# Optimization experiments

Measured on AMD Instinct MI355X. Metric: run time of the kernel, lower is better.

## Reference

```python
import jax, jax.numpy as jnp
import numpy as np

HC = 4
C = 2048
TMAX = 8
RMS_EPS = 1e-6
PRE_EPS = 1e-4
SINK_EPS = 1e-6
POST_MULT = 2.0


def setup_inputs() -> dict:
    key = jax.random.key(0)
    k1, k2, k3 = jax.random.split(key, 3)
    B, S = 2, 2048
    x = jax.random.normal(k1, (B, S, HC, C), dtype=jnp.float32)
    phi = jax.random.normal(k2, (HC * C, HC * HC + 2 * HC), dtype=jnp.float32) * 0.02
    b = jnp.zeros((HC * HC + 2 * HC,), dtype=jnp.float32)
    alpha_pre = jnp.ones((), dtype=jnp.float32)
    alpha_post = jnp.ones((), dtype=jnp.float32)
    alpha_res = jnp.ones((), dtype=jnp.float32)
    W = jax.random.normal(k3, (C, C), dtype=jnp.float32) * 0.02
    Wb = jnp.zeros((C,), dtype=jnp.float32)
    return {"x": x, "phi": phi, "b": b, "alpha_pre": alpha_pre,
            "alpha_post": alpha_post, "alpha_res": alpha_res, "W": W, "Wb": Wb}


def _coeffs(x, phi, b, alpha_pre, alpha_post, alpha_res):
    # x: [..., hc, c] -> flatten streams, RMSNorm over k = hc*c
    lead = x.shape[:-2]
    flat = x.reshape(lead + (HC * C,))
    xn = flat * jax.lax.rsqrt(jnp.mean(flat * flat, axis=-1, keepdims=True) + RMS_EPS)
    logits = xn @ phi + b  # [..., hc*hc + 2*hc]
    pre = logits[..., :HC]
    post = logits[..., HC:2 * HC]
    res = logits[..., 2 * HC:].reshape(lead + (HC, HC))
    h_pre = jax.nn.sigmoid(alpha_pre * pre) + PRE_EPS          # [..., hc]
    h_post = POST_MULT * jax.nn.sigmoid(alpha_post * post)     # [..., hc]
    # Sinkhorn normalization -> approximately doubly-stochastic hc x hc matrix
    M = jnp.exp(alpha_res * res)

    def step(m, _):
        m = m / (jnp.sum(m, axis=-1, keepdims=True) + SINK_EPS)
        m = m / (jnp.sum(m, axis=-2, keepdims=True) + SINK_EPS)
        return m, None

    h_res, _ = jax.lax.scan(step, M, None, length=TMAX)
    return h_pre, h_post, h_res


def reference(x, phi, b, alpha_pre, alpha_post, alpha_res, W, Wb):
    xf = x.astype(jnp.float32)
    h_pre, h_post, h_res = _coeffs(xf, phi, b, alpha_pre, alpha_post, alpha_res)
    # combine streams into single layer input: [..., c]
    x_in = jnp.sum(xf * h_pre[..., None], axis=-2)
    f_out = x_in @ W + Wb  # the wrapped layer (Linear)
    # residual stream mixing + broadcasted post-scaled layer output
    x_out = jnp.einsum('...oi,...ic->...oc', h_res, xf) + h_post[..., None] * f_out[..., None, :]
    return x_out.astype(x.dtype)
```

## Files before the change

kernel.cpp:

```cpp
#include <hip/hip_runtime.h>
#include <hip/hip_bf16.h>

#define HCn 4
#define Cn 2048
#define Dn (HCn*Cn)
#define NLg 24
#define TMAXn 8

typedef short bf16x8 __attribute__((ext_vector_type(8)));
typedef float f32x4 __attribute__((ext_vector_type(4)));

__device__ __forceinline__ unsigned int pk2(float a, float b) {
  union { __hip_bfloat162 h; unsigned int u; } v;
  v.h = __float22bfloat162_rn(float2{a, b});
  return v.u;
}
__device__ __forceinline__ unsigned short f2bfu(float a) {
  union { __hip_bfloat16 h; unsigned short u; } v;
  v.h = __float2bfloat16(a);
  return v.u;
}
__device__ __forceinline__ float bf2f(unsigned int u16) {
  union { float f; unsigned int x; } v;
  v.x = u16 << 16;
  return v.f;
}
__device__ __forceinline__ float sigm(float z) { return 1.0f / (1.0f + expf(-z)); }

__device__ __forceinline__ void gload_lds16(const void* g, void* l) {
  __builtin_amdgcn_global_load_lds((__attribute__((address_space(1))) void*)(g),
                                   (__attribute__((address_space(3))) void*)(l),
                                   16, 0, 0);
}

__global__ __launch_bounds__(128) void phib_kernel(const float* __restrict__ phi,
                                                   unsigned short* __restrict__ phiB) {
  int tid = threadIdx.x;
  int nt = tid >> 6, lane = tid & 63;
  int ks = blockIdx.x;
  int col = nt * 16 + (lane & 15);
  int kb = ks * 32 + (lane >> 4) * 8;
  float v[8];
#pragma unroll
  for (int e = 0; e < 8; ++e)
    v[e] = (col < NLg) ? phi[(size_t)(kb + e) * NLg + col] : 0.f;
  uint4 o = { pk2(v[0], v[1]), pk2(v[2], v[3]), pk2(v[4], v[5]), pk2(v[6], v[7]) };
  *(uint4*)&phiB[((size_t)(ks * 2 + nt) * 64 + lane) * 8] = o;
}

__global__ __launch_bounds__(512) void logits_kernel(
    const float* __restrict__ x, const unsigned short* __restrict__ phiB,
    float* __restrict__ pbuf) {
  __shared__ float lgp[8][16][33];
  __shared__ float ssp[8][16];

  int tid = threadIdx.x, lane = tid & 63, wid = tid >> 6;
  int g = blockIdx.x >> 2;
  int kc = blockIdx.x & 3;
  long t0 = (long)g * 16;
  int l15 = lane & 15, kg = lane >> 4;

  int kbase = kc * 2048 + wid * 256;
  const float* xr = x + (size_t)(t0 + l15) * Dn + kbase + kg * 8;
  const bf16x8* pB = (const bf16x8*)phiB + (size_t)(kbase >> 5) * 128 + lane;

  float ss = 0.f;
  f32x4 acc0 = {0.f,0.f,0.f,0.f}, acc1 = {0.f,0.f,0.f,0.f};

  float4 A0[3], A1[3]; bf16x8 Bv0[3], Bv1[3];
#define LOADIT(IT, S) {                          \
    A0[S] = *(const float4*)(xr + (IT) * 32);    \
    A1[S] = *(const float4*)(xr + (IT) * 32 + 4);\
    Bv0[S] = pB[(IT) * 128];                     \
    Bv1[S] = pB[(IT) * 128 + 64]; }
#define PROCIT(S) {                                                           \
    float4 P0 = A0[S], P1 = A1[S];                                            \
    ss += P0.x*P0.x + P0.y*P0.y + P0.z*P0.z + P0.w*P0.w;                      \
    ss += P1.x*P1.x + P1.y*P1.y + P1.z*P1.z + P1.w*P1.w;                      \
    uint4 u_ = { pk2(P0.x,P0.y), pk2(P0.z,P0.w), pk2(P1.x,P1.y), pk2(P1.z,P1.w) }; \
    bf16x8 a_ = *(bf16x8*)&u_;                                                \
    acc0 = __builtin_amdgcn_mfma_f32_16x16x32_bf16(a_, Bv0[S], acc0, 0, 0, 0);\
    acc1 = __builtin_amdgcn_mfma_f32_16x16x32_bf16(a_, Bv1[S], acc1, 0, 0, 0); }

  LOADIT(0, 0); LOADIT(1, 1);
#pragma unroll
  for (int it = 0; it < 8; ++it) {
    if (it < 6) LOADIT(it + 2, (it + 2) % 3);
    PROCIT(it % 3);
  }
#undef LOADIT
#undef PROCIT

  ss += __shfl_xor(ss, 16); ss += __shfl_xor(ss, 32);
  if (kg == 0) ssp[wid][l15] = ss;
#pragma unroll
  for (int e = 0; e < 4; ++e) {
    int tok = kg * 4 + e;
    lgp[wid][tok][l15] = acc0[e];
    lgp[wid][tok][16 + l15] = acc1[e];
  }
  __syncthreads();

  for (int q = tid; q < 16 * 25; q += 512) {
    int tk = q / 25, j = q % 25;
    float v = 0.f;
    if (j < 24) {
#pragma unroll
      for (int w = 0; w < 8; ++w) v += lgp[w][tk][j];
    } else {
#pragma unroll
      for (int w = 0; w < 8; ++w) v += ssp[w][tk];
    }
    pbuf[(size_t)(t0 + tk) * 100 + kc * 25 + j] = v;
  }
}

__global__ __launch_bounds__(256) void finalize_kernel(
    const float* __restrict__ pbuf, const float* __restrict__ bb,
    const float* __restrict__ apre_p, const float* __restrict__ apost_p,
    const float* __restrict__ ares_p, float* __restrict__ hpre,
    float* __restrict__ hpost, float* __restrict__ hres) {
  long t = (long)blockIdx.x * 256 + threadIdx.x;
  const float* pt = pbuf + (size_t)t * 100;
  float lg[25];
#pragma unroll
  for (int j = 0; j < 25; ++j)
    lg[j] = pt[j] + pt[25 + j] + pt[50 + j] + pt[75 + j];
  float r = rsqrtf(lg[24] / (float)Dn + 1e-6f);
  float apre = apre_p[0], apost = apost_p[0], ares = ares_p[0];
#pragma unroll
  for (int j = 0; j < NLg; ++j) lg[j] = r * lg[j] + bb[j];
#pragma unroll
  for (int j = 0; j < 4; ++j) hpre[t * 4 + j] = sigm(apre * lg[j]) + 1e-4f;
#pragma unroll
  for (int j = 0; j < 4; ++j) hpost[t * 4 + j] = 2.0f * sigm(apost * lg[4 + j]);
  float m[16];
#pragma unroll
  for (int q = 0; q < 16; ++q) m[q] = expf(ares * lg[8 + q]);
  for (int it = 0; it < TMAXn; ++it) {
#pragma unroll
    for (int o = 0; o < 4; ++o) {
      float rs = m[o*4] + m[o*4+1] + m[o*4+2] + m[o*4+3] + 1e-6f;
      m[o*4] /= rs; m[o*4+1] /= rs; m[o*4+2] /= rs; m[o*4+3] /= rs;
    }
#pragma unroll
    for (int i = 0; i < 4; ++i) {
      float cs = m[i] + m[4+i] + m[8+i] + m[12+i] + 1e-6f;
      m[i] /= cs; m[4+i] /= cs; m[8+i] /= cs; m[12+i] /= cs;
    }
  }
#pragma unroll
  for (int q = 0; q < 16; ++q) hres[t * 16 + q] = m[q];
}

__global__ __launch_bounds__(256) void xin_kernel(
    const float* __restrict__ x, const float* __restrict__ hpre,
    unsigned int* __restrict__ xin) {
  long t = blockIdx.x;
  int tid = threadIdx.x;
  float h0 = hpre[t * 4 + 0], h1 = hpre[t * 4 + 1];
  float h2 = hpre[t * 4 + 2], h3 = hpre[t * 4 + 3];
  const float4* xt = (const float4*)(x + (size_t)t * Dn);
  uint2* xo = (uint2*)xin + (size_t)t * (Cn / 4);
#pragma unroll
  for (int it = 0; it < 2; ++it) {
    int c4 = it * 256 + tid;
    float4 v0 = xt[c4];
    float4 v1 = xt[c4 + 512];
    float4 v2 = xt[c4 + 1024];
    float4 v3 = xt[c4 + 1536];
    float sx = h0*v0.x + h1*v1.x + h2*v2.x + h3*v3.x;
    float sy = h0*v0.y + h1*v1.y + h2*v2.y + h3*v3.y;
    float sz = h0*v0.z + h1*v1.z + h2*v2.z + h3*v3.z;
    float sw = h0*v0.w + h1*v1.w + h2*v2.w + h3*v3.w;
    uint2 o; o.x = pk2(sx, sy); o.y = pk2(sz, sw);
    xo[c4] = o;
  }
}

__global__ __launch_bounds__(256) void wtrans_kernel(const float* __restrict__ W,
                                                     unsigned short* __restrict__ Wt) {
  __shared__ float tile[64][65];
  int kb = blockIdx.y * 64, nb = blockIdx.x * 64;
  int tr = threadIdx.x >> 4;
  int tc = threadIdx.x & 15;
#pragma unroll
  for (int rr = 0; rr < 64; rr += 16) {
    float4 v = *(const float4*)&W[(size_t)(kb + tr + rr) * Cn + nb + tc * 4];
    tile[tr + rr][tc * 4 + 0] = v.x; tile[tr + rr][tc * 4 + 1] = v.y;
    tile[tr + rr][tc * 4 + 2] = v.z; tile[tr + rr][tc * 4 + 3] = v.w;
  }
  __syncthreads();
#pragma unroll
  for (int rr = 0; rr < 64; rr += 16) {
    int n = nb + tr + rr;
    uint2 o;
    o.x = pk2(tile[tc * 4 + 0][tr + rr], tile[tc * 4 + 1][tr + rr]);
    o.y = pk2(tile[tc * 4 + 2][tr + rr], tile[tc * 4 + 3][tr + rr]);
    *(uint2*)&Wt[(size_t)n * Cn + kb + tc * 4] = o;
  }
}

#define BMt 128
#define BNt 128
#define BKt 64
#define GK Cn
__global__ __launch_bounds__(256) void gemm_kernel(
    const unsigned short* __restrict__ xin, const unsigned short* __restrict__ Wt,
    const float* __restrict__ Wb, unsigned short* __restrict__ f) {
  __shared__ __align__(16) unsigned short As[2][BMt * BKt];
  __shared__ __align__(16) unsigned short Bs[2][BNt * BKt];
  int tid = threadIdx.x;
  int lane = tid & 63, wid = tid >> 6;
  int wr = wid >> 1, wc = wid & 1;
  int l15 = lane & 15, kg = lane >> 4;
  int wg = blockIdx.x;
  wg = (wg & 7) * 64 + (wg >> 3);
  int bx = wg & 15, by = wg >> 4;

  f32x4 acc[4][4];
#pragma unroll
  for (int i = 0; i < 4; ++i)
#pragma unroll
    for (int j = 0; j < 4; ++j) acc[i][j] = {0.f, 0.f, 0.f, 0.f};

  const char* Ab = (const char*)xin + (size_t)by * BMt * (GK * 2);
  const char* Bb = (const char*)Wt + (size_t)bx * BNt * (GK * 2);

  int soff[4]; size_t sgl[4];
#pragma unroll
  for (int i = 0; i < 4; ++i) {
    int off = tid * 16 + i * 4096;
    int row = off >> 7, col = off & 127;
    int scol = col ^ ((row & 7) << 4);
    soff[i] = off;
    sgl[i] = (size_t)row * (GK * 2) + scol;
  }
#define STAGEG(BUF, K0) {                                                      \
    _Pragma("unroll")                                                          \
    for (int i_ = 0; i_ < 4; ++i_)                                             \
      gload_lds16(Ab + sgl[i_] + (size_t)(K0) * 2, (char*)As[BUF] + soff[i_]); \
    _Pragma("unroll")                                                          \
    for (int i_ = 0; i_ < 4; ++i_)                                             \
      gload_lds16(Bb + sgl[i_] + (size_t)(K0) * 2, (char*)Bs[BUF] + soff[i_]); }

  int aoff[4][2], boff[4][2];
#pragma unroll
  for (int fm = 0; fm < 4; ++fm) {
    int ar = wr * 64 + fm * 16 + l15;
    int br = wc * 64 + fm * 16 + l15;
#pragma unroll
    for (int ks = 0; ks < 2; ++ks) {
      int c = ks * 64 + kg * 16;
      aoff[fm][ks] = ar * 128 + (c ^ ((ar & 7) << 4));
      boff[fm][ks] = br * 128 + (c ^ ((br & 7) << 4));
    }
  }

  STAGEG(0, 0);
  asm volatile("s_waitcnt vmcnt(0)" ::: "memory");
  __builtin_amdgcn_s_barrier();

  for (int t = 0; t < GK / BKt; ++t) {
    int cur = t & 1;
    if (t < GK / BKt - 1) STAGEG(cur ^ 1, (t + 1) * BKt);
#pragma unroll
    for (int ks = 0; ks < 2; ++ks) {
      bf16x8 av[4], bv[4];
#pragma unroll
      for (int fm = 0; fm < 4; ++fm)
        av[fm] = *(const bf16x8*)((const char*)As[cur] + aoff[fm][ks]);
#pragma unroll
      for (int fn = 0; fn < 4; ++fn)
        bv[fn] = *(const bf16x8*)((const char*)Bs[cur] + boff[fn][ks]);
#pragma unroll
      for (int fm = 0; fm < 4; ++fm)
#pragma unroll
        for (int fn = 0; fn < 4; ++fn)
          acc[fm][fn] = __builtin_amdgcn_mfma_f32_16x16x32_bf16(av[fm], bv[fn], acc[fm][fn], 0, 0, 0);
    }
    asm volatile("s_waitcnt vmcnt(0)" ::: "memory");
    __builtin_amdgcn_s_barrier();
  }

  int m0 = by * BMt + wr * 64;
  int n0 = bx * BNt + wc * 64;
#pragma unroll
  for (int fm = 0; fm < 4; ++fm) {
#pragma unroll
    for (int e = 0; e < 4; ++e) {
      int t = m0 + fm * 16 + kg * 4 + e;
      unsigned short* ft = f + (size_t)t * Cn;
#pragma unroll
      for (int fn = 0; fn < 4; ++fn) {
        int c = n0 + fn * 16 + l15;
        ft[c] = f2bfu(acc[fm][fn][e] + Wb[c]);
      }
    }
  }
}

__global__ __launch_bounds__(256) void epilogue_kernel(
    const float* __restrict__ x, const unsigned short* __restrict__ f,
    const float* __restrict__ hpost, const float* __restrict__ hres,
    float* __restrict__ out) {
  long t = blockIdx.x;
  int tid = threadIdx.x;
  float hq[4], hr[16];
#pragma unroll
  for (int o = 0; o < 4; ++o) hq[o] = hpost[t * 4 + o];
#pragma unroll
  for (int q = 0; q < 16; ++q) hr[q] = hres[t * 16 + q];
  const float4* xt = (const float4*)(x + (size_t)t * Dn);
  const uint2* ft = (const uint2*)(f + (size_t)t * Cn);
  float* ot = out + (size_t)t * Dn;
#pragma unroll
  for (int it = 0; it < 2; ++it) {
    int c4 = it * 256 + tid;
    float4 x0 = xt[c4], x1 = xt[c4 + 512], x2 = xt[c4 + 1024], x3 = xt[c4 + 1536];
    uint2 fu = ft[c4];
    float4 fv = { bf2f(fu.x & 0xffffu), bf2f(fu.x >> 16),
                  bf2f(fu.y & 0xffffu), bf2f(fu.y >> 16) };
#pragma unroll
    for (int o = 0; o < 4; ++o) {
      float a = hr[o*4+0], b = hr[o*4+1], c = hr[o*4+2], d = hr[o*4+3], q = hq[o];
      f32x4 r;
      r[0] = q*fv.x + a*x0.x + b*x1.x + c*x2.x + d*x3.x;
      r[1] = q*fv.y + a*x0.y + b*x1.y + c*x2.y + d*x3.y;
      r[2] = q*fv.z + a*x0.z + b*x1.z + c*x2.z + d*x3.z;
      r[3] = q*fv.w + a*x0.w + b*x1.w + c*x2.w + d*x3.w;
      __builtin_nontemporal_store(r, (f32x4*)&ot[(size_t)o * Cn + c4 * 4]);
    }
  }
}

extern "C" void kernel_launch(void* const* d_in, const int* in_sizes, int n_in,
                              void* d_out, int out_size, void* d_ws, size_t ws_size,
                              hipStream_t stream) {
  const float* x     = (const float*)d_in[0];
  const float* phi   = (const float*)d_in[1];
  const float* b     = (const float*)d_in[2];
  const float* apre  = (const float*)d_in[3];
  const float* apost = (const float*)d_in[4];
  const float* ares  = (const float*)d_in[5];
  const float* W     = (const float*)d_in[6];
  const float* Wb    = (const float*)d_in[7];
  float* out = (float*)d_out;

  int NT = in_sizes[0] / Dn;
  char* ws = (char*)d_ws;
  size_t off = 0;
  unsigned int*   xin  = (unsigned int*)(ws + off);   off += (size_t)NT * Cn * 2;
  unsigned short* Wt   = (unsigned short*)(ws + off); off += (size_t)Cn * Cn * 2;
  float* hpre  = (float*)(ws + off); off += (size_t)NT * 4 * 4;
  float* hpost = (float*)(ws + off); off += (size_t)NT * 4 * 4;
  float* hres  = (float*)(ws + off); off += (size_t)NT * 16 * 4;
  unsigned short* phiB = (unsigned short*)(ws + off); off += (size_t)Dn * 32 * 2;
  float* pbuf  = (float*)(ws + off); off += (size_t)NT * 100 * 4;
  unsigned short* fbuf = (unsigned short*)(ws + off); off += (size_t)NT * Cn * 2;

  hipLaunchKernelGGL(phib_kernel, dim3(Dn / 32), dim3(128), 0, stream, phi, phiB);
  hipLaunchKernelGGL(logits_kernel, dim3((NT / 16) * 4), dim3(512), 0, stream,
                     x, phiB, pbuf);
  hipLaunchKernelGGL(finalize_kernel, dim3(NT / 256), dim3(256), 0, stream,
                     pbuf, b, apre, apost, ares, hpre, hpost, hres);
  hipLaunchKernelGGL(xin_kernel, dim3(NT), dim3(256), 0, stream, x, hpre, xin);
  hipLaunchKernelGGL(wtrans_kernel, dim3(Cn / 64, Cn / 64), dim3(256), 0, stream, W, Wt);
  hipLaunchKernelGGL(gemm_kernel, dim3((Cn / BNt) * (NT / BMt)), dim3(256), 0, stream,
                     (const unsigned short*)xin, Wt, Wb, fbuf);
  hipLaunchKernelGGL(epilogue_kernel, dim3(NT), dim3(256), 0, stream,
                     x, fbuf, hpost, hres, out);
}
```

Before: 164.2 us.

## Stage x tiles through LDS with async global-to-LDS loads in logits kernel

The logits kernel now moves x into a per-wave double-buffered LDS area using direct global-to-LDS 16-byte loads, instead of prefetching into registers three stages deep. It synchronises with explicit vmcnt/lgkmcnt waits and scheduling barriers. All eight phi fragments are loaded into registers up front rather than streamed alongside x. The aim is to cut register pressure and keep more memory traffic in flight while the bf16 conversion and MFMA run. In exchange it adds an LDS round trip, hand-written wait counts that must match the load order, and extra registers for the preloaded B fragments.

```diff
diff --git a/kernel.cpp b/kernel.cpp
--- a/kernel.cpp
+++ b/kernel.cpp
@@ -51,6 +51,7 @@
 __global__ __launch_bounds__(512) void logits_kernel(
     const float* __restrict__ x, const unsigned short* __restrict__ phiB,
     float* __restrict__ pbuf) {
+  __shared__ __align__(16) float Axs[8][2][512];
   __shared__ float lgp[8][16][33];
   __shared__ float ssp[8][16];
 
@@ -58,44 +59,62 @@
   int g = blockIdx.x >> 2;
   int kc = blockIdx.x & 3;
   long t0 = (long)g * 16;
-  int l15 = lane & 15, kg = lane >> 4;
-
-  int kbase = kc * 2048 + wid * 256;
-  const float* xr = x + (size_t)(t0 + l15) * Dn + kbase + kg * 8;
-  const bf16x8* pB = (const bf16x8*)phiB + (size_t)(kbase >> 5) * 128 + lane;
+  int l15 = lane & 15, sg = lane >> 4;
+
+  int kwin = kc * 2048 + wid * 256;
+  const float* xs = x + (size_t)(t0 + l15) * Dn + kwin + sg * 8;
+  const bf16x8* pB = (const bf16x8*)phiB + (size_t)(kwin >> 5) * 128 + lane;
+
+  float* A0 = &Axs[wid][0][0];
+  float* A1 = &Axs[wid][1][0];
+
+  bf16x8 Bv0[8], Bv1[8];
+#pragma unroll
+  for (int it = 0; it < 8; ++it) {
+    Bv0[it] = pB[it * 128];
+    Bv1[it] = pB[it * 128 + 64];
+  }
+
+#define STAGE(IT, BUF) {                                                 \
+    gload_lds16(xs + (IT) * 32,     (char*)(BUF) + lane * 16);           \
+    gload_lds16(xs + (IT) * 32 + 4, (char*)(BUF) + 1024 + lane * 16); }
+
+  int rb0 = l15 * 16 + sg * 256;
+  int rb1 = rb0 + 1024;
 
   float ss = 0.f;
   f32x4 acc0 = {0.f,0.f,0.f,0.f}, acc1 = {0.f,0.f,0.f,0.f};
 
-  float4 A0[3], A1[3]; bf16x8 Bv0[3], Bv1[3];
-#define LOADIT(IT, S) {                          \
-    A0[S] = *(const float4*)(xr + (IT) * 32);    \
-    A1[S] = *(const float4*)(xr + (IT) * 32 + 4);\
-    Bv0[S] = pB[(IT) * 128];                     \
-    Bv1[S] = pB[(IT) * 128 + 64]; }
-#define PROCIT(S) {                                                           \
-    float4 P0 = A0[S], P1 = A1[S];                                            \
-    ss += P0.x*P0.x + P0.y*P0.y + P0.z*P0.z + P0.w*P0.w;                      \
-    ss += P1.x*P1.x + P1.y*P1.y + P1.z*P1.z + P1.w*P1.w;                      \
-    uint4 u_ = { pk2(P0.x,P0.y), pk2(P0.z,P0.w), pk2(P1.x,P1.y), pk2(P1.z,P1.w) }; \
-    bf16x8 a_ = *(bf16x8*)&u_;                                                \
-    acc0 = __builtin_amdgcn_mfma_f32_16x16x32_bf16(a_, Bv0[S], acc0, 0, 0, 0);\
-    acc1 = __builtin_amdgcn_mfma_f32_16x16x32_bf16(a_, Bv1[S], acc1, 0, 0, 0); }
-
-  LOADIT(0, 0); LOADIT(1, 1);
+  STAGE(0, A0);
+  STAGE(1, A1);
 #pragma unroll
   for (int it = 0; it < 8; ++it) {
-    if (it < 6) LOADIT(it + 2, (it + 2) % 3);
-    PROCIT(it % 3);
-  }
-#undef LOADIT
-#undef PROCIT
+    float* cb = (it & 1) ? A1 : A0;
+    if (it < 7) {
+      asm volatile("s_waitcnt vmcnt(2)" ::: "memory");
+    } else {
+      asm volatile("s_waitcnt vmcnt(0)" ::: "memory");
+    }
+    __builtin_amdgcn_sched_barrier(0);
+    float4 a0 = *(const float4*)((const char*)cb + rb0);
+    float4 a1 = *(const float4*)((const char*)cb + rb1);
+    asm volatile("s_waitcnt lgkmcnt(0)" ::: "memory");
+    __builtin_amdgcn_sched_barrier(0);
+    if (it < 6) STAGE(it + 2, cb);
+    ss += a0.x*a0.x + a0.y*a0.y + a0.z*a0.z + a0.w*a0.w;
+    ss += a1.x*a1.x + a1.y*a1.y + a1.z*a1.z + a1.w*a1.w;
+    uint4 u_ = { pk2(a0.x,a0.y), pk2(a0.z,a0.w), pk2(a1.x,a1.y), pk2(a1.z,a1.w) };
+    bf16x8 a_ = *(bf16x8*)&u_;
+    acc0 = __builtin_amdgcn_mfma_f32_16x16x32_bf16(a_, Bv0[it], acc0, 0, 0, 0);
+    acc1 = __builtin_amdgcn_mfma_f32_16x16x32_bf16(a_, Bv1[it], acc1, 0, 0, 0);
+  }
+#undef STAGE
 
   ss += __shfl_xor(ss, 16); ss += __shfl_xor(ss, 32);
-  if (kg == 0) ssp[wid][l15] = ss;
+  if (sg == 0) ssp[wid][l15] = ss;
 #pragma unroll
   for (int e = 0; e < 4; ++e) {
-    int tok = kg * 4 + e;
+    int tok = sg * 4 + e;
     lgp[wid][tok][l15] = acc0[e];
     lgp[wid][tok][16 + l15] = acc1[e];
   }
```

Result: no change. 165.1 us (+0.6%).

## Fuse logits, finalize and stream-combine into one coeffs kernel staging x in LDS

Applied to the files above, without the earlier changes.

Replaces the logits, finalize and xin kernels with a single kernel that handles 4 tokens per block. The block loads each token's row of x once, stores it as bf16 in shared memory, and reuses that copy for the RMS norm, the phi MFMA and the h_pre-weighted stream combine. This removes the second global read of x in xin_kernel, the pbuf round trip and two launches. In exchange, x_in is now computed from bf16-rounded x rather than fp32, which adds error. Each block also uses about 66KB of LDS and only 4 of the 16 MFMA rows carry real tokens, so occupancy is lower and MFMA work is wasted.

```diff
diff --git a/kernel.cpp b/kernel.cpp
--- a/kernel.cpp
+++ b/kernel.cpp
@@ -6,6 +6,7 @@
 #define Dn (HCn*Cn)
 #define NLg 24
 #define TMAXn 8
+#define TSx 8240
 
 typedef short bf16x8 __attribute__((ext_vector_type(8)));
 typedef float f32x4 __attribute__((ext_vector_type(4)));
@@ -48,133 +49,134 @@
   *(uint4*)&phiB[((size_t)(ks * 2 + nt) * 64 + lane) * 8] = o;
 }
 
-__global__ __launch_bounds__(512) void logits_kernel(
+__global__ __launch_bounds__(512) void coeffs_kernel(
     const float* __restrict__ x, const unsigned short* __restrict__ phiB,
-    float* __restrict__ pbuf) {
-  __shared__ float lgp[8][16][33];
-  __shared__ float ssp[8][16];
+    const float* __restrict__ bb, const float* __restrict__ apre_p,
+    const float* __restrict__ apost_p, const float* __restrict__ ares_p,
+    unsigned int* __restrict__ xin, float* __restrict__ hpost,
+    float* __restrict__ hres) {
+  __shared__ __align__(16) unsigned short xls[4 * TSx];
+  __shared__ float lgp[8][4][33];
+  __shared__ float ssw[8][4];
+  __shared__ float hpre_s[4][4];
 
   int tid = threadIdx.x, lane = tid & 63, wid = tid >> 6;
-  int g = blockIdx.x >> 2;
-  int kc = blockIdx.x & 3;
-  long t0 = (long)g * 16;
-  int l15 = lane & 15, kg = lane >> 4;
-
-  int kbase = kc * 2048 + wid * 256;
-  const float* xr = x + (size_t)(t0 + l15) * Dn + kbase + kg * 8;
-  const bf16x8* pB = (const bf16x8*)phiB + (size_t)(kbase >> 5) * 128 + lane;
-
-  float ss = 0.f;
-  f32x4 acc0 = {0.f,0.f,0.f,0.f}, acc1 = {0.f,0.f,0.f,0.f};
-
-  float4 A0[3], A1[3]; bf16x8 Bv0[3], Bv1[3];
-#define LOADIT(IT, S) {                          \
-    A0[S] = *(const float4*)(xr + (IT) * 32);    \
-    A1[S] = *(const float4*)(xr + (IT) * 32 + 4);\
-    Bv0[S] = pB[(IT) * 128];                     \
-    Bv1[S] = pB[(IT) * 128 + 64]; }
-#define PROCIT(S) {                                                           \
-    float4 P0 = A0[S], P1 = A1[S];                                            \
-    ss += P0.x*P0.x + P0.y*P0.y + P0.z*P0.z + P0.w*P0.w;                      \
-    ss += P1.x*P1.x + P1.y*P1.y + P1.z*P1.z + P1.w*P1.w;                      \
-    uint4 u_ = { pk2(P0.x,P0.y), pk2(P0.z,P0.w), pk2(P1.x,P1.y), pk2(P1.z,P1.w) }; \
-    bf16x8 a_ = *(bf16x8*)&u_;                                                \
-    acc0 = __builtin_amdgcn_mfma_f32_16x16x32_bf16(a_, Bv0[S], acc0, 0, 0, 0);\
-    acc1 = __builtin_amdgcn_mfma_f32_16x16x32_bf16(a_, Bv1[S], acc1, 0, 0, 0); }
-
-  LOADIT(0, 0); LOADIT(1, 1);
-#pragma unroll
-  for (int it = 0; it < 8; ++it) {
-    if (it < 6) LOADIT(it + 2, (it + 2) % 3);
-    PROCIT(it % 3);
-  }
-#undef LOADIT
-#undef PROCIT
-
-  ss += __shfl_xor(ss, 16); ss += __shfl_xor(ss, 32);
-  if (kg == 0) ssp[wid][l15] = ss;
-#pragma unroll
-  for (int e = 0; e < 4; ++e) {
-    int tok = kg * 4 + e;
-    lgp[wid][tok][l15] = acc0[e];
-    lgp[wid][tok][16 + l15] = acc1[e];
+  long t0 = (long)blockIdx.x * 4;
+  const float4* xb = (const float4*)(x + (size_t)t0 * Dn);
+
+  float ss[4] = {0.f, 0.f, 0.f, 0.f};
+#pragma unroll
+  for (int p = 0; p < 8; ++p) {
+    int idx = p * 4096 + tid * 8;
+    int tok = p >> 1;
+    int ch = idx & 8191;
+    float4 v0 = xb[idx >> 2];
+    float4 v1 = xb[(idx >> 2) + 1];
+    ss[tok] += v0.x*v0.x + v0.y*v0.y + v0.z*v0.z + v0.w*v0.w
+             + v1.x*v1.x + v1.y*v1.y + v1.z*v1.z + v1.w*v1.w;
+    uint4 u = { pk2(v0.x,v0.y), pk2(v0.z,v0.w), pk2(v1.x,v1.y), pk2(v1.z,v1.w) };
+    *(uint4*)&xls[tok * TSx + ch] = u;
+  }
+#pragma unroll
+  for (int j = 0; j < 4; ++j) {
+    float s = ss[j];
+    s += __shfl_xor(s, 1);  s += __shfl_xor(s, 2);  s += __shfl_xor(s, 4);
+    s += __shfl_xor(s, 8);  s += __shfl_xor(s, 16); s += __shfl_xor(s, 32);
+    if (lane == 0) ssw[wid][j] = s;
   }
   __syncthreads();
 
-  for (int q = tid; q < 16 * 25; q += 512) {
-    int tk = q / 25, j = q % 25;
-    float v = 0.f;
-    if (j < 24) {
-#pragma unroll
-      for (int w = 0; w < 8; ++w) v += lgp[w][tk][j];
-    } else {
-#pragma unroll
-      for (int w = 0; w < 8; ++w) v += ssp[w][tk];
-    }
-    pbuf[(size_t)(t0 + tk) * 100 + kc * 25 + j] = v;
-  }
-}
-
-__global__ __launch_bounds__(256) void finalize_kernel(
-    const float* __restrict__ pbuf, const float* __restrict__ bb,
-    const float* __restrict__ apre_p, const float* __restrict__ apost_p,
-    const float* __restrict__ ares_p, float* __restrict__ hpre,
-    float* __restrict__ hpost, float* __restrict__ hres) {
-  long t = (long)blockIdx.x * 256 + threadIdx.x;
-  const float* pt = pbuf + (size_t)t * 100;
-  float lg[25];
-#pragma unroll
-  for (int j = 0; j < 25; ++j)
-    lg[j] = pt[j] + pt[25 + j] + pt[50 + j] + pt[75 + j];
-  float r = rsqrtf(lg[24] / (float)Dn + 1e-6f);
-  float apre = apre_p[0], apost = apost_p[0], ares = ares_p[0];
-#pragma unroll
-  for (int j = 0; j < NLg; ++j) lg[j] = r * lg[j] + bb[j];
-#pragma unroll
-  for (int j = 0; j < 4; ++j) hpre[t * 4 + j] = sigm(apre * lg[j]) + 1e-4f;
-#pragma unroll
-  for (int j = 0; j < 4; ++j) hpost[t * 4 + j] = 2.0f * sigm(apost * lg[4 + j]);
-  float m[16];
-#pragma unroll
-  for (int q = 0; q < 16; ++q) m[q] = expf(ares * lg[8 + q]);
-  for (int it = 0; it < TMAXn; ++it) {
-#pragma unroll
-    for (int o = 0; o < 4; ++o) {
-      float rs = m[o*4] + m[o*4+1] + m[o*4+2] + m[o*4+3] + 1e-6f;
-      m[o*4] /= rs; m[o*4+1] /= rs; m[o*4+2] /= rs; m[o*4+3] /= rs;
-    }
-#pragma unroll
-    for (int i = 0; i < 4; ++i) {
-      float cs = m[i] + m[4+i] + m[8+i] + m[12+i] + 1e-6f;
-      m[i] /= cs; m[4+i] /= cs; m[8+i] /= cs; m[12+i] /= cs;
-    }
-  }
-#pragma unroll
-  for (int q = 0; q < 16; ++q) hres[t * 16 + q] = m[q];
-}
-
-__global__ __launch_bounds__(256) void xin_kernel(
-    const float* __restrict__ x, const float* __restrict__ hpre,
-    unsigned int* __restrict__ xin) {
-  long t = blockIdx.x;
-  int tid = threadIdx.x;
-  float h0 = hpre[t * 4 + 0], h1 = hpre[t * 4 + 1];
-  float h2 = hpre[t * 4 + 2], h3 = hpre[t * 4 + 3];
-  const float4* xt = (const float4*)(x + (size_t)t * Dn);
-  uint2* xo = (uint2*)xin + (size_t)t * (Cn / 4);
-#pragma unroll
-  for (int it = 0; it < 2; ++it) {
-    int c4 = it * 256 + tid;
-    float4 v0 = xt[c4];
-    float4 v1 = xt[c4 + 512];
-    float4 v2 = xt[c4 + 1024];
-    float4 v3 = xt[c4 + 1536];
-    float sx = h0*v0.x + h1*v1.x + h2*v2.x + h3*v3.x;
-    float sy = h0*v0.y + h1*v1.y + h2*v2.y + h3*v3.y;
-    float sz = h0*v0.z + h1*v1.z + h2*v2.z + h3*v3.z;
-    float sw = h0*v0.w + h1*v1.w + h2*v2.w + h3*v3.w;
-    uint2 o; o.x = pk2(sx, sy); o.y = pk2(sz, sw);
-    xo[c4] = o;
+  {
+    int l15 = lane & 15, sg = lane >> 4;
+    const unsigned short* arow = &xls[(l15 & 3) * TSx];
+    int kwin = wid * 1024;
+    const bf16x8* pB = (const bf16x8*)phiB + (size_t)(kwin >> 5) * 128 + lane;
+    f32x4 acc0 = {0.f,0.f,0.f,0.f}, acc1 = {0.f,0.f,0.f,0.f};
+#pragma unroll
+    for (int it = 0; it < 32; ++it) {
+      int k = kwin + it * 32 + sg * 8;
+      bf16x8 a = *(const bf16x8*)&arow[k];
+      bf16x8 b0 = pB[it * 128];
+      bf16x8 b1 = pB[it * 128 + 64];
+      acc0 = __builtin_amdgcn_mfma_f32_16x16x32_bf16(a, b0, acc0, 0, 0, 0);
+      acc1 = __builtin_amdgcn_mfma_f32_16x16x32_bf16(a, b1, acc1, 0, 0, 0);
+    }
+    if (sg == 0) {
+#pragma unroll
+      for (int e = 0; e < 4; ++e) {
+        lgp[wid][e][l15] = acc0[e];
+        lgp[wid][e][16 + l15] = acc1[e];
+      }
+    }
+  }
+  __syncthreads();
+
+  if (tid < 4) {
+    long t = t0 + tid;
+    float st = 0.f;
+#pragma unroll
+    for (int w = 0; w < 8; ++w) st += ssw[w][tid];
+    float r = rsqrtf(st / (float)Dn + 1e-6f);
+    float apre = apre_p[0], apost = apost_p[0], ares = ares_p[0];
+    float lg[NLg];
+#pragma unroll
+    for (int j = 0; j < NLg; ++j) {
+      float d = 0.f;
+#pragma unroll
+      for (int w = 0; w < 8; ++w) d += lgp[w][tid][j];
+      lg[j] = r * d + bb[j];
+    }
+#pragma unroll
+    for (int j = 0; j < 4; ++j) hpre_s[tid][j] = sigm(apre * lg[j]) + 1e-4f;
+#pragma unroll
+    for (int j = 0; j < 4; ++j) hpost[t * 4 + j] = 2.0f * sigm(apost * lg[4 + j]);
+    float m[16];
+#pragma unroll
+    for (int q = 0; q < 16; ++q) m[q] = expf(ares * lg[8 + q]);
+    for (int it = 0; it < TMAXn; ++it) {
+#pragma unroll
+      for (int o = 0; o < 4; ++o) {
+        float rs = m[o*4] + m[o*4+1] + m[o*4+2] + m[o*4+3] + 1e-6f;
+        m[o*4] /= rs; m[o*4+1] /= rs; m[o*4+2] /= rs; m[o*4+3] /= rs;
+      }
+#pragma unroll
+      for (int i = 0; i < 4; ++i) {
+        float cs = m[i] + m[4+i] + m[8+i] + m[12+i] + 1e-6f;
+        m[i] /= cs; m[4+i] /= cs; m[8+i] /= cs; m[12+i] /= cs;
+      }
+    }
+#pragma unroll
+    for (int q = 0; q < 16; ++q) hres[t * 16 + q] = m[q];
+  }
+  __syncthreads();
+
+  {
+    int tk = tid >> 7;
+    int c0 = (tid & 127) * 16;
+    float h0 = hpre_s[tk][0], h1 = hpre_s[tk][1], h2 = hpre_s[tk][2], h3 = hpre_s[tk][3];
+    float s[16];
+#pragma unroll
+    for (int i = 0; i < 16; ++i) s[i] = 0.f;
+#pragma unroll
+    for (int hc = 0; hc < 4; ++hc) {
+      float h = (hc == 0) ? h0 : (hc == 1) ? h1 : (hc == 2) ? h2 : h3;
+      int base = tk * TSx + hc * 2048 + c0;
+      uint4 u0 = *(const uint4*)&xls[base];
+      uint4 u1 = *(const uint4*)&xls[base + 8];
+      s[0]  += h * bf2f(u0.x & 0xffffu); s[1]  += h * bf2f(u0.x >> 16);
+      s[2]  += h * bf2f(u0.y & 0xffffu); s[3]  += h * bf2f(u0.y >> 16);
+      s[4]  += h * bf2f(u0.z & 0xffffu); s[5]  += h * bf2f(u0.z >> 16);
+      s[6]  += h * bf2f(u0.w & 0xffffu); s[7]  += h * bf2f(u0.w >> 16);
+      s[8]  += h * bf2f(u1.x & 0xffffu); s[9]  += h * bf2f(u1.x >> 16);
+      s[10] += h * bf2f(u1.y & 0xffffu); s[11] += h * bf2f(u1.y >> 16);
+      s[12] += h * bf2f(u1.z & 0xffffu); s[13] += h * bf2f(u1.z >> 16);
+      s[14] += h * bf2f(u1.w & 0xffffu); s[15] += h * bf2f(u1.w >> 16);
+    }
+    unsigned short* xo = (unsigned short*)xin + ((size_t)(t0 + tk) * Cn + c0);
+    uint4 o0 = { pk2(s[0], s[1]),  pk2(s[2], s[3]),  pk2(s[4], s[5]),  pk2(s[6], s[7]) };
+    uint4 o1 = { pk2(s[8], s[9]),  pk2(s[10],s[11]), pk2(s[12],s[13]), pk2(s[14],s[15]) };
+    *(uint4*)&xo[0] = o0;
+    *(uint4*)&xo[8] = o1;
   }
 }
 
@@ -352,19 +354,14 @@
   size_t off = 0;
   unsigned int*   xin  = (unsigned int*)(ws + off);   off += (size_t)NT * Cn * 2;
   unsigned short* Wt   = (unsigned short*)(ws + off); off += (size_t)Cn * Cn * 2;
-  float* hpre  = (float*)(ws + off); off += (size_t)NT * 4 * 4;
   float* hpost = (float*)(ws + off); off += (size_t)NT * 4 * 4;
   float* hres  = (float*)(ws + off); off += (size_t)NT * 16 * 4;
   unsigned short* phiB = (unsigned short*)(ws + off); off += (size_t)Dn * 32 * 2;
-  float* pbuf  = (float*)(ws + off); off += (size_t)NT * 100 * 4;
   unsigned short* fbuf = (unsigned short*)(ws + off); off += (size_t)NT * Cn * 2;
 
   hipLaunchKernelGGL(phib_kernel, dim3(Dn / 32), dim3(128), 0, stream, phi, phiB);
-  hipLaunchKernelGGL(logits_kernel, dim3((NT / 16) * 4), dim3(512), 0, stream,
-                     x, phiB, pbuf);
-  hipLaunchKernelGGL(finalize_kernel, dim3(NT / 256), dim3(256), 0, stream,
-                     pbuf, b, apre, apost, ares, hpre, hpost, hres);
-  hipLaunchKernelGGL(xin_kernel, dim3(NT), dim3(256), 0, stream, x, hpre, xin);
+  hipLaunchKernelGGL(coeffs_kernel, dim3(NT / 4), dim3(512), 0, stream,
+                     x, phiB, b, apre, apost, ares, xin, hpost, hres);
   hipLaunchKernelGGL(wtrans_kernel, dim3(Cn / 64, Cn / 64), dim3(256), 0, stream, W, Wt);
   hipLaunchKernelGGL(gemm_kernel, dim3((Cn / BNt) * (NT / BMt)), dim3(256), 0, stream,
                      (const unsigned short*)xin, Wt, Wb, fbuf);
```

Result: no change. 165.7 us (+0.9%).

## Transcode x to bf16 once and feed all downstream kernels from it

Applied to the files above, without the earlier changes.

Adds a transcode kernel that converts x to bf16 once and computes the per-token sum of squares. The logits, xin and epilogue kernels then read the half-size bf16 copy instead of fp32 x, and logits no longer computes the RMS partials itself. The aim is to cut bytes read across the three x consumers. In exchange it adds a full fp32 read plus a bf16 write and one more launch, so total memory traffic stays about the same. It also lowers the residual mixing term in the output to bf16 inputs, which costs accuracy.

```diff
diff --git a/kernel.cpp b/kernel.cpp
--- a/kernel.cpp
+++ b/kernel.cpp
@@ -25,6 +25,12 @@
   v.x = u16 << 16;
   return v.f;
 }
+__device__ __forceinline__ void unpack8(uint4 v, float* o) {
+  o[0] = bf2f(v.x & 0xffffu); o[1] = bf2f(v.x >> 16);
+  o[2] = bf2f(v.y & 0xffffu); o[3] = bf2f(v.y >> 16);
+  o[4] = bf2f(v.z & 0xffffu); o[5] = bf2f(v.z >> 16);
+  o[6] = bf2f(v.w & 0xffffu); o[7] = bf2f(v.w >> 16);
+}
 __device__ __forceinline__ float sigm(float z) { return 1.0f / (1.0f + expf(-z)); }
 
 __device__ __forceinline__ void gload_lds16(const void* g, void* l) {
@@ -48,39 +54,54 @@
   *(uint4*)&phiB[((size_t)(ks * 2 + nt) * 64 + lane) * 8] = o;
 }
 
+__global__ __launch_bounds__(256) void transcode_kernel(
+    const float* __restrict__ x, unsigned short* __restrict__ xbf,
+    float* __restrict__ ssbuf) {
+  long t = blockIdx.x;
+  int tid = threadIdx.x;
+  const float4* xt = (const float4*)(x + (size_t)t * Dn);
+  uint2* xo = (uint2*)(xbf + (size_t)t * Dn);
+  float ss = 0.f;
+#pragma unroll
+  for (int i = 0; i < 8; ++i) {
+    float4 v = xt[i * 256 + tid];
+    ss += v.x*v.x + v.y*v.y + v.z*v.z + v.w*v.w;
+    uint2 o; o.x = pk2(v.x, v.y); o.y = pk2(v.z, v.w);
+    xo[i * 256 + tid] = o;
+  }
+  ss += __shfl_xor(ss, 1);  ss += __shfl_xor(ss, 2);  ss += __shfl_xor(ss, 4);
+  ss += __shfl_xor(ss, 8);  ss += __shfl_xor(ss, 16); ss += __shfl_xor(ss, 32);
+  __shared__ float sred[4];
+  if ((tid & 63) == 0) sred[tid >> 6] = ss;
+  __syncthreads();
+  if (tid == 0) ssbuf[t] = sred[0] + sred[1] + sred[2] + sred[3];
+}
+
 __global__ __launch_bounds__(512) void logits_kernel(
-    const float* __restrict__ x, const unsigned short* __restrict__ phiB,
+    const unsigned short* __restrict__ xbf, const unsigned short* __restrict__ phiB,
     float* __restrict__ pbuf) {
   __shared__ float lgp[8][16][33];
-  __shared__ float ssp[8][16];
 
   int tid = threadIdx.x, lane = tid & 63, wid = tid >> 6;
   int g = blockIdx.x >> 2;
   int kc = blockIdx.x & 3;
   long t0 = (long)g * 16;
-  int l15 = lane & 15, kg = lane >> 4;
+  int l15 = lane & 15, sg = lane >> 4;
 
   int kbase = kc * 2048 + wid * 256;
-  const float* xr = x + (size_t)(t0 + l15) * Dn + kbase + kg * 8;
+  const unsigned short* xr = xbf + (size_t)(t0 + l15) * Dn + kbase + sg * 8;
   const bf16x8* pB = (const bf16x8*)phiB + (size_t)(kbase >> 5) * 128 + lane;
 
-  float ss = 0.f;
   f32x4 acc0 = {0.f,0.f,0.f,0.f}, acc1 = {0.f,0.f,0.f,0.f};
 
-  float4 A0[3], A1[3]; bf16x8 Bv0[3], Bv1[3];
+  bf16x8 Av[3], Bv0[3], Bv1[3];
 #define LOADIT(IT, S) {                          \
-    A0[S] = *(const float4*)(xr + (IT) * 32);    \
-    A1[S] = *(const float4*)(xr + (IT) * 32 + 4);\
+    Av[S]  = *(const bf16x8*)(xr + (IT) * 32);   \
     Bv0[S] = pB[(IT) * 128];                     \
     Bv1[S] = pB[(IT) * 128 + 64]; }
-#define PROCIT(S) {                                                           \
-    float4 P0 = A0[S], P1 = A1[S];                                            \
-    ss += P0.x*P0.x + P0.y*P0.y + P0.z*P0.z + P0.w*P0.w;                      \
-    ss += P1.x*P1.x + P1.y*P1.y + P1.z*P1.z + P1.w*P1.w;                      \
-    uint4 u_ = { pk2(P0.x,P0.y), pk2(P0.z,P0.w), pk2(P1.x,P1.y), pk2(P1.z,P1.w) }; \
-    bf16x8 a_ = *(bf16x8*)&u_;                                                \
-    acc0 = __builtin_amdgcn_mfma_f32_16x16x32_bf16(a_, Bv0[S], acc0, 0, 0, 0);\
-    acc1 = __builtin_amdgcn_mfma_f32_16x16x32_bf16(a_, Bv1[S], acc1, 0, 0, 0); }
+#define PROCIT(S) {                                                            \
+    acc0 = __builtin_amdgcn_mfma_f32_16x16x32_bf16(Av[S], Bv0[S], acc0, 0, 0, 0); \
+    acc1 = __builtin_amdgcn_mfma_f32_16x16x32_bf16(Av[S], Bv1[S], acc1, 0, 0, 0); }
 
   LOADIT(0, 0); LOADIT(1, 1);
 #pragma unroll
@@ -91,42 +112,35 @@
 #undef LOADIT
 #undef PROCIT
 
-  ss += __shfl_xor(ss, 16); ss += __shfl_xor(ss, 32);
-  if (kg == 0) ssp[wid][l15] = ss;
 #pragma unroll
   for (int e = 0; e < 4; ++e) {
-    int tok = kg * 4 + e;
+    int tok = sg * 4 + e;
     lgp[wid][tok][l15] = acc0[e];
     lgp[wid][tok][16 + l15] = acc1[e];
   }
   __syncthreads();
 
-  for (int q = tid; q < 16 * 25; q += 512) {
-    int tk = q / 25, j = q % 25;
+  for (int q = tid; q < 16 * 24; q += 512) {
+    int tk = q / 24, j = q % 24;
     float v = 0.f;
-    if (j < 24) {
-#pragma unroll
-      for (int w = 0; w < 8; ++w) v += lgp[w][tk][j];
-    } else {
-#pragma unroll
-      for (int w = 0; w < 8; ++w) v += ssp[w][tk];
-    }
-    pbuf[(size_t)(t0 + tk) * 100 + kc * 25 + j] = v;
+#pragma unroll
+    for (int w = 0; w < 8; ++w) v += lgp[w][tk][j];
+    pbuf[(size_t)(t0 + tk) * 96 + kc * 24 + j] = v;
   }
 }
 
 __global__ __launch_bounds__(256) void finalize_kernel(
-    const float* __restrict__ pbuf, const float* __restrict__ bb,
-    const float* __restrict__ apre_p, const float* __restrict__ apost_p,
-    const float* __restrict__ ares_p, float* __restrict__ hpre,
-    float* __restrict__ hpost, float* __restrict__ hres) {
+    const float* __restrict__ pbuf, const float* __restrict__ ssbuf,
+    const float* __restrict__ bb, const float* __restrict__ apre_p,
+    const float* __restrict__ apost_p, const float* __restrict__ ares_p,
+    float* __restrict__ hpre, float* __restrict__ hpost, float* __restrict__ hres) {
   long t = (long)blockIdx.x * 256 + threadIdx.x;
-  const float* pt = pbuf + (size_t)t * 100;
-  float lg[25];
-#pragma unroll
-  for (int j = 0; j < 25; ++j)
-    lg[j] = pt[j] + pt[25 + j] + pt[50 + j] + pt[75 + j];
-  float r = rsqrtf(lg[24] / (float)Dn + 1e-6f);
+  const float* pt = pbuf + (size_t)t * 96;
+  float lg[NLg];
+#pragma unroll
+  for (int j = 0; j < NLg; ++j)
+    lg[j] = pt[j] + pt[24 + j] + pt[48 + j] + pt[72 + j];
+  float r = rsqrtf(ssbuf[t] / (float)Dn + 1e-6f);
   float apre = apre_p[0], apost = apost_p[0], ares = ares_p[0];
 #pragma unroll
   for (int j = 0; j < NLg; ++j) lg[j] = r * lg[j] + bb[j];
@@ -154,28 +168,21 @@
 }
 
 __global__ __launch_bounds__(256) void xin_kernel(
-    const float* __restrict__ x, const float* __restrict__ hpre,
+    const unsigned short* __restrict__ xbf, const float* __restrict__ hpre,
     unsigned int* __restrict__ xin) {
   long t = blockIdx.x;
   int tid = threadIdx.x;
   float h0 = hpre[t * 4 + 0], h1 = hpre[t * 4 + 1];
   float h2 = hpre[t * 4 + 2], h3 = hpre[t * 4 + 3];
-  const float4* xt = (const float4*)(x + (size_t)t * Dn);
-  uint2* xo = (uint2*)xin + (size_t)t * (Cn / 4);
-#pragma unroll
-  for (int it = 0; it < 2; ++it) {
-    int c4 = it * 256 + tid;
-    float4 v0 = xt[c4];
-    float4 v1 = xt[c4 + 512];
-    float4 v2 = xt[c4 + 1024];
-    float4 v3 = xt[c4 + 1536];
-    float sx = h0*v0.x + h1*v1.x + h2*v2.x + h3*v3.x;
-    float sy = h0*v0.y + h1*v1.y + h2*v2.y + h3*v3.y;
-    float sz = h0*v0.z + h1*v1.z + h2*v2.z + h3*v3.z;
-    float sw = h0*v0.w + h1*v1.w + h2*v2.w + h3*v3.w;
-    uint2 o; o.x = pk2(sx, sy); o.y = pk2(sz, sw);
-    xo[c4] = o;
-  }
+  const uint4* xb = (const uint4*)(xbf + (size_t)t * Dn);
+  uint4 v0 = xb[tid], v1 = xb[256 + tid], v2 = xb[512 + tid], v3 = xb[768 + tid];
+  float X0[8], X1[8], X2[8], X3[8];
+  unpack8(v0, X0); unpack8(v1, X1); unpack8(v2, X2); unpack8(v3, X3);
+  float s[8];
+#pragma unroll
+  for (int e = 0; e < 8; ++e) s[e] = h0*X0[e] + h1*X1[e] + h2*X2[e] + h3*X3[e];
+  uint4 o = { pk2(s[0], s[1]), pk2(s[2], s[3]), pk2(s[4], s[5]), pk2(s[6], s[7]) };
+  ((uint4*)xin)[(size_t)t * 256 + tid] = o;
 }
 
 __global__ __launch_bounds__(256) void wtrans_kernel(const float* __restrict__ W,
@@ -301,7 +308,7 @@
 }
 
 __global__ __launch_bounds__(256) void epilogue_kernel(
-    const float* __restrict__ x, const unsigned short* __restrict__ f,
+    const unsigned short* __restrict__ xbf, const unsigned short* __restrict__ f,
     const float* __restrict__ hpost, const float* __restrict__ hres,
     float* __restrict__ out) {
   long t = blockIdx.x;
@@ -311,26 +318,26 @@
   for (int o = 0; o < 4; ++o) hq[o] = hpost[t * 4 + o];
 #pragma unroll
   for (int q = 0; q < 16; ++q) hr[q] = hres[t * 16 + q];
-  const float4* xt = (const float4*)(x + (size_t)t * Dn);
-  const uint2* ft = (const uint2*)(f + (size_t)t * Cn);
+  const uint4* xb = (const uint4*)(xbf + (size_t)t * Dn);
+  const uint4* fb = (const uint4*)(f + (size_t)t * Cn);
   float* ot = out + (size_t)t * Dn;
-#pragma unroll
-  for (int it = 0; it < 2; ++it) {
-    int c4 = it * 256 + tid;
-    float4 x0 = xt[c4], x1 = xt[c4 + 512], x2 = xt[c4 + 1024], x3 = xt[c4 + 1536];
-    uint2 fu = ft[c4];
-    float4 fv = { bf2f(fu.x & 0xffffu), bf2f(fu.x >> 16),
-                  bf2f(fu.y & 0xffffu), bf2f(fu.y >> 16) };
-#pragma unroll
-    for (int o = 0; o < 4; ++o) {
-      float a = hr[o*4+0], b = hr[o*4+1], c = hr[o*4+2], d = hr[o*4+3], q = hq[o];
-      f32x4 r;
-      r[0] = q*fv.x + a*x0.x + b*x1.x + c*x2.x + d*x3.x;
-      r[1] = q*fv.y + a*x0.y + b*x1.y + c*x2.y + d*x3.y;
-      r[2] = q*fv.z + a*x0.z + b*x1.z + c*x2.z + d*x3.z;
-      r[3] = q*fv.w + a*x0.w + b*x1.w + c*x2.w + d*x3.w;
-      __builtin_nontemporal_store(r, (f32x4*)&ot[(size_t)o * Cn + c4 * 4]);
-    }
+
+  uint4 v0 = xb[tid], v1 = xb[256 + tid], v2 = xb[512 + tid], v3 = xb[768 + tid];
+  uint4 fv = fb[tid];
+  float X0[8], X1[8], X2[8], X3[8], F[8];
+  unpack8(v0, X0); unpack8(v1, X1); unpack8(v2, X2); unpack8(v3, X3);
+  unpack8(fv, F);
+#pragma unroll
+  for (int o = 0; o < 4; ++o) {
+    float a = hr[o*4+0], b = hr[o*4+1], c = hr[o*4+2], d = hr[o*4+3], q = hq[o];
+    float r[8];
+#pragma unroll
+    for (int e = 0; e < 8; ++e)
+      r[e] = q*F[e] + a*X0[e] + b*X1[e] + c*X2[e] + d*X3[e];
+    f32x4 r0 = { r[0], r[1], r[2], r[3] };
+    f32x4 r1 = { r[4], r[5], r[6], r[7] };
+    __builtin_nontemporal_store(r0, (f32x4*)&ot[(size_t)o * Cn + tid * 8]);
+    __builtin_nontemporal_store(r1, (f32x4*)&ot[(size_t)o * Cn + tid * 8 + 4]);
   }
 }
 
@@ -350,24 +357,27 @@
   int NT = in_sizes[0] / Dn;
   char* ws = (char*)d_ws;
   size_t off = 0;
+  unsigned short* xbf  = (unsigned short*)(ws + off); off += (size_t)NT * Dn * 2;
   unsigned int*   xin  = (unsigned int*)(ws + off);   off += (size_t)NT * Cn * 2;
   unsigned short* Wt   = (unsigned short*)(ws + off); off += (size_t)Cn * Cn * 2;
+  unsigned short* fbuf = (unsigned short*)(ws + off); off += (size_t)NT * Cn * 2;
   float* hpre  = (float*)(ws + off); off += (size_t)NT * 4 * 4;
   float* hpost = (float*)(ws + off); off += (size_t)NT * 4 * 4;
   float* hres  = (float*)(ws + off); off += (size_t)NT * 16 * 4;
+  float* ssbuf = (float*)(ws + off); off += (size_t)NT * 4;
   unsigned short* phiB = (unsigned short*)(ws + off); off += (size_t)Dn * 32 * 2;
-  float* pbuf  = (float*)(ws + off); off += (size_t)NT * 100 * 4;
-  unsigned short* fbuf = (unsigned short*)(ws + off); off += (size_t)NT * Cn * 2;
+  float* pbuf  = (float*)(ws + off); off += (size_t)NT * 96 * 4;
 
   hipLaunchKernelGGL(phib_kernel, dim3(Dn / 32), dim3(128), 0, stream, phi, phiB);
+  hipLaunchKernelGGL(transcode_kernel, dim3(NT), dim3(256), 0, stream, x, xbf, ssbuf);
   hipLaunchKernelGGL(logits_kernel, dim3((NT / 16) * 4), dim3(512), 0, stream,
-                     x, phiB, pbuf);
+                     xbf, phiB, pbuf);
   hipLaunchKernelGGL(finalize_kernel, dim3(NT / 256), dim3(256), 0, stream,
-                     pbuf, b, apre, apost, ares, hpre, hpost, hres);
-  hipLaunchKernelGGL(xin_kernel, dim3(NT), dim3(256), 0, stream, x, hpre, xin);
+                     pbuf, ssbuf, b, apre, apost, ares, hpre, hpost, hres);
+  hipLaunchKernelGGL(xin_kernel, dim3(NT), dim3(256), 0, stream, xbf, hpre, xin);
   hipLaunchKernelGGL(wtrans_kernel, dim3(Cn / 64, Cn / 64), dim3(256), 0, stream, W, Wt);
   hipLaunchKernelGGL(gemm_kernel, dim3((Cn / BNt) * (NT / BMt)), dim3(256), 0, stream,
                      (const unsigned short*)xin, Wt, Wb, fbuf);
   hipLaunchKernelGGL(epilogue_kernel, dim3(NT), dim3(256), 0, stream,
-                     x, fbuf, hpost, hres, out);
-}
+                     xbf, fbuf, hpost, hres, out);
+}
```

Measured after the change: 184.4 us. 12.3% more time.
